# Optimization experiments

Measured on AMD Instinct MI355X. Metric: run time of the kernel, lower is better.

Reference implementation:

```python
import jax, jax.numpy as jnp
import numpy as np

B, N, NAB, NF, NG = 2, 512, 128, 128, 32
CUTOFF = 5.0


def ssp(x):
    # shifted softplus: ln(1+e^x) - ln 2
    return jax.nn.softplus(x) - jnp.log(2.0).astype(x.dtype)


def setup_inputs() -> dict:
    key = jax.random.key(0)
    ks = jax.random.split(key, 10)
    offsets = jnp.linspace(0.0, CUTOFF, NG)
    widths = jnp.full((NG,), offsets[1] - offsets[0])
    s = 0.05
    return {
        "r": jax.random.normal(ks[0], (B, N, NAB), jnp.float32),
        "e": jax.random.uniform(ks[1], (B, N, N), jnp.float32),
        "A": jax.random.uniform(ks[2], (B, N, N), jnp.float32),
        "offsets": offsets,
        "widths": widths,
        "W_df1": jax.random.normal(ks[3], (NG, NG), jnp.float32) * s,
        "b_df1": jnp.zeros((NG,), jnp.float32),
        "W_df2": jax.random.normal(ks[4], (NG, NF), jnp.float32) * s,
        "b_df2": jnp.zeros((NF,), jnp.float32),
        "W_af": jax.random.normal(ks[5], (NAB, NF), jnp.float32) * s,
        "W_d1": jax.random.normal(ks[6], (NF, NAB), jnp.float32) * s,
        "b_d1": jnp.zeros((NAB,), jnp.float32),
        "W_d2": jax.random.normal(ks[7], (NAB, NAB), jnp.float32) * s,
        "b_d2": jnp.zeros((NAB,), jnp.float32),
    }


def reference(r, e, A, offsets, widths, W_df1, b_df1, W_df2, b_df2,
              W_af, W_d1, b_d1, W_d2, b_d2):
    # Gaussian smearing (trainable offsets/widths, non-centered)
    coeff = -0.5 / (widths ** 2)                       # [G]
    diff = e[:, :, :, None] - offsets[None, None, None, :]  # [B,N,N,G]
    es = jnp.exp(coeff * diff ** 2)                    # [B,N,N,G]
    # DistanceFilter1 output is computed then discarded (faithful to source)
    _ = ssp(es @ W_df1 + b_df1)
    W = es @ W_df2 + b_df2                             # [B,N,N,F]
    rf = r @ W_af                                      # [B,N,F]
    # cfconv: broadcast-multiply-reduce over neighbor axis j
    y = jnp.einsum("bjf,bij,bijf->bif", rf, A, W)      # [B,N,F]
    y = ssp(y @ W_d1 + b_d1)                           # [B,N,NAB]
    y = y @ W_d2 + b_d2                                # [B,N,NAB]
    return y
```

## Files before the change

kernel.cpp:

```cpp
#include <hip/hip_runtime.h>
#include <math.h>

#define BB 2
#define NN 512
#define NAB 128
#define NF 128
#define NG 32

typedef _Float16 f16;
typedef f16 f16x8 __attribute__((ext_vector_type(8)));
typedef f16 f16x4 __attribute__((ext_vector_type(4)));
typedef f16 f16x2 __attribute__((ext_vector_type(2)));
typedef float f32x4 __attribute__((ext_vector_type(4)));

#define TS 520
#define SS 132

__global__ __launch_bounds__(256) void prep_rf(const float* __restrict__ r,
                                               const float* __restrict__ W_af,
                                               const float* __restrict__ W_d1,
                                               const float* __restrict__ W_d2,
                                               f16* __restrict__ rfT,
                                               f16* __restrict__ W1T,
                                               f16* __restrict__ W2T) {
    const int tid = threadIdx.x;
    const int r0  = blockIdx.x * 2;
    const int b   = r0 >> 9;
    const int j0  = r0 & 511;

    if (blockIdx.x < 32) {
        const int m  = blockIdx.x >> 4;
        const float* Wsrc = m ? W_d2 : W_d1;
        f16* Wdst = m ? W2T : W1T;
        const int k0 = (blockIdx.x & 15) * 8 + (tid >> 7) * 4;
        const int f  = tid & 127;
        f16x4 v;
        #pragma unroll
        for (int t = 0; t < 4; ++t) v[t] = (f16)Wsrc[(k0 + t) * NAB + f];
        *(f16x4*)(Wdst + f * NAB + k0) = v;
    }

    __shared__ float sr[2][128];
    __shared__ f16   st[128][2];

    if (tid < 256) {
        const int rr = tid >> 7, ff = tid & 127;
        sr[rr][ff] = r[(r0 + rr) * NAB + ff];
    }
    __syncthreads();

    const int f  = tid & 127;
    const int rh = tid >> 7;
    float a0 = 0.f;
    #pragma unroll 8
    for (int k = 0; k < NAB; ++k)
        a0 += sr[rh][k] * W_af[k * NF + f];
    st[f][rh] = (f16)a0;
    __syncthreads();

    if (tid < 128)
        *(f16x2*)(rfT + b * (NF * NN) + tid * NN + j0) = *(f16x2*)st[tid];
}

__global__ __launch_bounds__(256, 4) void fused_kernel(
    const float* __restrict__ e, const float* __restrict__ A,
    const f16*  __restrict__ rfT,
    const f16*  __restrict__ W1T, const f16* __restrict__ W2T,
    const float* __restrict__ offsets, const float* __restrict__ widths,
    const float* __restrict__ W_df2, const float* __restrict__ b_df2,
    const float* __restrict__ b_d1,  const float* __restrict__ b_d2,
    float* __restrict__ out) {

    const int bi  = blockIdx.x;
    const int b   = bi >> 9;
    const int tid = threadIdx.x;
    const int w    = tid >> 6;
    const int lane = tid & 63;
    const int q    = lane >> 4;
    const int n    = lane & 15;

    __shared__ __align__(16) float smem[2 * 33 * SS];
    __shared__ float sconst[64];
    __shared__ float sh1[128];
    __shared__ __align__(16) f16 yh16[128];
    __shared__ __align__(16) f16 hh16[128];

    f16* Tsh = (f16*)smem;

    if (tid < NG) {
        sconst[tid] = offsets[tid];
        const float wd = widths[tid];
        sconst[32 + tid] = -0.5f / (wd * wd);
    }

    const int j0 = (tid & 127) * 4;
    const float4 ev = *(const float4*)(e + bi * NN + j0);
    const float4 av = *(const float4*)(A + bi * NN + j0);
    __syncthreads();

    #pragma unroll
    for (int i = 0; i < 16; ++i) {
        const int g = (tid >> 7) + 2 * i;
        const float off = sconst[g];
        const float cf  = sconst[32 + g];
        const float d0 = ev.x - off, d1 = ev.y - off;
        const float d2 = ev.z - off, d3 = ev.w - off;
        f16x4 v;
        v[0] = (f16)(av.x * __expf(cf * d0 * d0));
        v[1] = (f16)(av.y * __expf(cf * d1 * d1));
        v[2] = (f16)(av.z * __expf(cf * d2 * d2));
        v[3] = (f16)(av.w * __expf(cf * d3 * d3));
        *(f16x4*)(Tsh + g * TS + j0) = v;
    }
    if (tid < 128) {
        f16x4 v;
        v[0] = (f16)av.x; v[1] = (f16)av.y; v[2] = (f16)av.z; v[3] = (f16)av.w;
        *(f16x4*)(Tsh + 32 * TS + j0) = v;
    }
    __syncthreads();

    const int kh = w >> 1;
    const int nh = w & 1;

    f32x4 acc[3][4];
    #pragma unroll
    for (int mt = 0; mt < 3; ++mt)
        #pragma unroll
        for (int nt = 0; nt < 4; ++nt)
            acc[mt][nt] = (f32x4){0.f, 0.f, 0.f, 0.f};

    const f16* Abase  = Tsh + n * TS + kh * 256 + q * 8;
    const f16* A2base = Tsh + 32 * TS + kh * 256 + q * 8;
    const f16* Bbase  = rfT + (size_t)b * (NF * NN) + (nh * 64 + n) * NN + kh * 256 + q * 8;

    #pragma unroll
    for (int kk = 0; kk < 8; ++kk) {
        f16x8 bc[4];
        #pragma unroll
        for (int nt = 0; nt < 4; ++nt)
            bc[nt] = *(const f16x8*)(Bbase + kk * 32 + nt * 16 * NN);
        const f16x8 a0 = *(const f16x8*)(Abase + kk * 32);
        const f16x8 a1 = *(const f16x8*)(Abase + 16 * TS + kk * 32);
        const f16x8 a2 = *(const f16x8*)(A2base + kk * 32);
        #pragma unroll
        for (int nt = 0; nt < 4; ++nt) {
            acc[0][nt] = __builtin_amdgcn_mfma_f32_16x16x32_f16(a0, bc[nt], acc[0][nt], 0, 0, 0);
            acc[1][nt] = __builtin_amdgcn_mfma_f32_16x16x32_f16(a1, bc[nt], acc[1][nt], 0, 0, 0);
            acc[2][nt] = __builtin_amdgcn_mfma_f32_16x16x32_f16(a2, bc[nt], acc[2][nt], 0, 0, 0);
        }
    }

    __syncthreads();
    float* Sp = smem + kh * (33 * SS);
    #pragma unroll
    for (int mt = 0; mt < 2; ++mt)
        #pragma unroll
        for (int nt = 0; nt < 4; ++nt)
            #pragma unroll
            for (int rr = 0; rr < 4; ++rr)
                Sp[(mt * 16 + q * 4 + rr) * SS + nh * 64 + nt * 16 + n] = acc[mt][nt][rr];
    if (q == 0) {
        #pragma unroll
        for (int nt = 0; nt < 4; ++nt)
            Sp[32 * SS + nh * 64 + nt * 16 + n] = acc[2][nt][0];
    }
    __syncthreads();

    if (tid < 128) {
        const float* S0 = smem;
        const float* S1 = smem + 33 * SS;
        float a = b_df2[tid] * (S0[32 * SS + tid] + S1[32 * SS + tid]);
        #pragma unroll 8
        for (int g = 0; g < NG; ++g)
            a += W_df2[g * NF + tid] * (S0[g * SS + tid] + S1[g * SS + tid]);
        yh16[tid] = (f16)a;
    }
    __syncthreads();

    f32x4 m1[2];
    m1[0] = (f32x4){0.f, 0.f, 0.f, 0.f};
    m1[1] = (f32x4){0.f, 0.f, 0.f, 0.f};
    #pragma unroll
    for (int kk = 0; kk < 4; ++kk) {
        const f16x8 af = *(const f16x8*)(yh16 + kk * 32 + q * 8);
        #pragma unroll
        for (int nt = 0; nt < 2; ++nt) {
            const f16x8 bf = *(const f16x8*)(W1T + (w * 32 + nt * 16 + n) * NAB + kk * 32 + q * 8);
            m1[nt] = __builtin_amdgcn_mfma_f32_16x16x32_f16(af, bf, m1[nt], 0, 0, 0);
        }
    }
    if (lane < 16) {
        sh1[w * 32 + 0  + lane] = m1[0][0];
        sh1[w * 32 + 16 + lane] = m1[1][0];
    }
    __syncthreads();

    if (tid < 128) {
        const float x = sh1[tid] + b_d1[tid];
        const float sp = (x > 0.f) ? (x + log1pf(__expf(-x))) : log1pf(__expf(x));
        hh16[tid] = (f16)(sp - 0.69314718055994530942f);
    }
    __syncthreads();

    f32x4 m2[2];
    m2[0] = (f32x4){0.f, 0.f, 0.f, 0.f};
    m2[1] = (f32x4){0.f, 0.f, 0.f, 0.f};
    #pragma unroll
    for (int kk = 0; kk < 4; ++kk) {
        const f16x8 af = *(const f16x8*)(hh16 + kk * 32 + q * 8);
        #pragma unroll
        for (int nt = 0; nt < 2; ++nt) {
            const f16x8 bf = *(const f16x8*)(W2T + (w * 32 + nt * 16 + n) * NAB + kk * 32 + q * 8);
            m2[nt] = __builtin_amdgcn_mfma_f32_16x16x32_f16(af, bf, m2[nt], 0, 0, 0);
        }
    }
    if (lane < 16) {
        const int f0 = w * 32 + lane;
        out[bi * NAB + f0]      = m2[0][0] + b_d2[f0];
        out[bi * NAB + f0 + 16] = m2[1][0] + b_d2[f0 + 16];
    }
}

extern "C" void kernel_launch(void* const* d_in, const int* in_sizes, int n_in,
                              void* d_out, int out_size, void* d_ws, size_t ws_size,
                              hipStream_t stream) {
    const float* r       = (const float*)d_in[0];
    const float* e       = (const float*)d_in[1];
    const float* A       = (const float*)d_in[2];
    const float* offsets = (const float*)d_in[3];
    const float* widths  = (const float*)d_in[4];
    const float* W_df2   = (const float*)d_in[7];
    const float* b_df2   = (const float*)d_in[8];
    const float* W_af    = (const float*)d_in[9];
    const float* W_d1    = (const float*)d_in[10];
    const float* b_d1    = (const float*)d_in[11];
    const float* W_d2    = (const float*)d_in[12];
    const float* b_d2    = (const float*)d_in[13];
    float* out = (float*)d_out;

    f16* rfT = (f16*)d_ws;
    f16* W1T = rfT + BB * NF * NN;
    f16* W2T = W1T + NAB * NAB;

    prep_rf<<<BB * NN / 2, 256, 0, stream>>>(r, W_af, W_d1, W_d2, rfT, W1T, W2T);
    fused_kernel<<<BB * NN, 256, 0, stream>>>(e, A, rfT, W1T, W2T,
                                              offsets, widths, W_df2, b_df2,
                                              b_d1, b_d2, out);
}
```

Before: 111.5 us.

## Process two atom rows per block to reuse rfT B-fragments

Each block of the fused kernel now handles two consecutive atoms i, sharing the rfT operand loads from global memory across both rows' MFMA accumulations and doubling the per-block weight reuse in the dense layers. The grid halves to 512 blocks and LDS doubles, with launch bounds relaxed to 2 blocks per CU. This trades occupancy and register pressure (96 accumulator vectors) for fewer global B loads and more MFMA work per load.

```diff
diff --git a/kernel.cpp b/kernel.cpp
--- a/kernel.cpp
+++ b/kernel.cpp
@@ -43,7 +43,7 @@
     __shared__ float sr[2][128];
     __shared__ f16   st[128][2];
 
-    if (tid < 256) {
+    {
         const int rr = tid >> 7, ff = tid & 127;
         sr[rr][ff] = r[(r0 + rr) * NAB + ff];
     }
@@ -62,7 +62,7 @@
         *(f16x2*)(rfT + b * (NF * NN) + tid * NN + j0) = *(f16x2*)st[tid];
 }
 
-__global__ __launch_bounds__(256, 4) void fused_kernel(
+__global__ __launch_bounds__(256, 2) void fused_kernel(
     const float* __restrict__ e, const float* __restrict__ A,
     const f16*  __restrict__ rfT,
     const f16*  __restrict__ W1T, const f16* __restrict__ W2T,
@@ -71,21 +71,22 @@
     const float* __restrict__ b_d1,  const float* __restrict__ b_d2,
     float* __restrict__ out) {
 
-    const int bi  = blockIdx.x;
-    const int b   = bi >> 9;
+    const int gi0 = blockIdx.x * 2;
+    const int b   = gi0 >> 9;
     const int tid = threadIdx.x;
     const int w    = tid >> 6;
     const int lane = tid & 63;
     const int q    = lane >> 4;
     const int n    = lane & 15;
 
-    __shared__ __align__(16) float smem[2 * 33 * SS];
+    __shared__ __align__(16) float smem[4 * 33 * SS];
     __shared__ float sconst[64];
-    __shared__ float sh1[128];
-    __shared__ __align__(16) f16 yh16[128];
-    __shared__ __align__(16) f16 hh16[128];
-
-    f16* Tsh = (f16*)smem;
+    __shared__ float sh1[2][128];
+    __shared__ __align__(16) f16 yh16[2][128];
+    __shared__ __align__(16) f16 hh16[2][128];
+
+    f16* Tsh0 = (f16*)smem;
+    f16* Tsh1 = Tsh0 + 33 * TS;
 
     if (tid < NG) {
         sconst[tid] = offsets[tid];
@@ -94,43 +95,63 @@
     }
 
     const int j0 = (tid & 127) * 4;
-    const float4 ev = *(const float4*)(e + bi * NN + j0);
-    const float4 av = *(const float4*)(A + bi * NN + j0);
-    __syncthreads();
-
-    #pragma unroll
-    for (int i = 0; i < 16; ++i) {
-        const int g = (tid >> 7) + 2 * i;
+    const float4 ev0 = *(const float4*)(e + (size_t)gi0 * NN + j0);
+    const float4 av0 = *(const float4*)(A + (size_t)gi0 * NN + j0);
+    const float4 ev1 = *(const float4*)(e + (size_t)(gi0 + 1) * NN + j0);
+    const float4 av1 = *(const float4*)(A + (size_t)(gi0 + 1) * NN + j0);
+    __syncthreads();
+
+    #pragma unroll
+    for (int it = 0; it < 16; ++it) {
+        const int g = (tid >> 7) + 2 * it;
         const float off = sconst[g];
         const float cf  = sconst[32 + g];
-        const float d0 = ev.x - off, d1 = ev.y - off;
-        const float d2 = ev.z - off, d3 = ev.w - off;
-        f16x4 v;
-        v[0] = (f16)(av.x * __expf(cf * d0 * d0));
-        v[1] = (f16)(av.y * __expf(cf * d1 * d1));
-        v[2] = (f16)(av.z * __expf(cf * d2 * d2));
-        v[3] = (f16)(av.w * __expf(cf * d3 * d3));
-        *(f16x4*)(Tsh + g * TS + j0) = v;
+        {
+            const float d0 = ev0.x - off, d1 = ev0.y - off;
+            const float d2 = ev0.z - off, d3 = ev0.w - off;
+            f16x4 v;
+            v[0] = (f16)(av0.x * __expf(cf * d0 * d0));
+            v[1] = (f16)(av0.y * __expf(cf * d1 * d1));
+            v[2] = (f16)(av0.z * __expf(cf * d2 * d2));
+            v[3] = (f16)(av0.w * __expf(cf * d3 * d3));
+            *(f16x4*)(Tsh0 + g * TS + j0) = v;
+        }
+        {
+            const float d0 = ev1.x - off, d1 = ev1.y - off;
+            const float d2 = ev1.z - off, d3 = ev1.w - off;
+            f16x4 v;
+            v[0] = (f16)(av1.x * __expf(cf * d0 * d0));
+            v[1] = (f16)(av1.y * __expf(cf * d1 * d1));
+            v[2] = (f16)(av1.z * __expf(cf * d2 * d2));
+            v[3] = (f16)(av1.w * __expf(cf * d3 * d3));
+            *(f16x4*)(Tsh1 + g * TS + j0) = v;
+        }
     }
     if (tid < 128) {
-        f16x4 v;
-        v[0] = (f16)av.x; v[1] = (f16)av.y; v[2] = (f16)av.z; v[3] = (f16)av.w;
-        *(f16x4*)(Tsh + 32 * TS + j0) = v;
+        f16x4 v0, v1;
+        v0[0] = (f16)av0.x; v0[1] = (f16)av0.y; v0[2] = (f16)av0.z; v0[3] = (f16)av0.w;
+        v1[0] = (f16)av1.x; v1[1] = (f16)av1.y; v1[2] = (f16)av1.z; v1[3] = (f16)av1.w;
+        *(f16x4*)(Tsh0 + 32 * TS + j0) = v0;
+        *(f16x4*)(Tsh1 + 32 * TS + j0) = v1;
     }
     __syncthreads();
 
     const int kh = w >> 1;
     const int nh = w & 1;
 
-    f32x4 acc[3][4];
-    #pragma unroll
-    for (int mt = 0; mt < 3; ++mt)
-        #pragma unroll
-        for (int nt = 0; nt < 4; ++nt)
-            acc[mt][nt] = (f32x4){0.f, 0.f, 0.f, 0.f};
-
-    const f16* Abase  = Tsh + n * TS + kh * 256 + q * 8;
-    const f16* A2base = Tsh + 32 * TS + kh * 256 + q * 8;
+    f32x4 acc[2][3][4];
+    #pragma unroll
+    for (int ii = 0; ii < 2; ++ii)
+        #pragma unroll
+        for (int mt = 0; mt < 3; ++mt)
+            #pragma unroll
+            for (int nt = 0; nt < 4; ++nt)
+                acc[ii][mt][nt] = (f32x4){0.f, 0.f, 0.f, 0.f};
+
+    const f16* A0base = Tsh0 + n * TS + kh * 256 + q * 8;
+    const f16* A0brow = Tsh0 + 32 * TS + kh * 256 + q * 8;
+    const f16* A1base = Tsh1 + n * TS + kh * 256 + q * 8;
+    const f16* A1brow = Tsh1 + 32 * TS + kh * 256 + q * 8;
     const f16* Bbase  = rfT + (size_t)b * (NF * NN) + (nh * 64 + n) * NN + kh * 256 + q * 8;
 
     #pragma unroll
@@ -139,85 +160,114 @@
         #pragma unroll
         for (int nt = 0; nt < 4; ++nt)
             bc[nt] = *(const f16x8*)(Bbase + kk * 32 + nt * 16 * NN);
-        const f16x8 a0 = *(const f16x8*)(Abase + kk * 32);
-        const f16x8 a1 = *(const f16x8*)(Abase + 16 * TS + kk * 32);
-        const f16x8 a2 = *(const f16x8*)(A2base + kk * 32);
+        const f16x8 a00 = *(const f16x8*)(A0base + kk * 32);
+        const f16x8 a01 = *(const f16x8*)(A0base + 16 * TS + kk * 32);
+        const f16x8 a02 = *(const f16x8*)(A0brow + kk * 32);
+        const f16x8 a10 = *(const f16x8*)(A1base + kk * 32);
+        const f16x8 a11 = *(const f16x8*)(A1base + 16 * TS + kk * 32);
+        const f16x8 a12 = *(const f16x8*)(A1brow + kk * 32);
         #pragma unroll
         for (int nt = 0; nt < 4; ++nt) {
-            acc[0][nt] = __builtin_amdgcn_mfma_f32_16x16x32_f16(a0, bc[nt], acc[0][nt], 0, 0, 0);
-            acc[1][nt] = __builtin_amdgcn_mfma_f32_16x16x32_f16(a1, bc[nt], acc[1][nt], 0, 0, 0);
-            acc[2][nt] = __builtin_amdgcn_mfma_f32_16x16x32_f16(a2, bc[nt], acc[2][nt], 0, 0, 0);
-        }
-    }
-
-    __syncthreads();
-    float* Sp = smem + kh * (33 * SS);
-    #pragma unroll
-    for (int mt = 0; mt < 2; ++mt)
-        #pragma unroll
-        for (int nt = 0; nt < 4; ++nt)
+            acc[0][0][nt] = __builtin_amdgcn_mfma_f32_16x16x32_f16(a00, bc[nt], acc[0][0][nt], 0, 0, 0);
+            acc[0][1][nt] = __builtin_amdgcn_mfma_f32_16x16x32_f16(a01, bc[nt], acc[0][1][nt], 0, 0, 0);
+            acc[0][2][nt] = __builtin_amdgcn_mfma_f32_16x16x32_f16(a02, bc[nt], acc[0][2][nt], 0, 0, 0);
+            acc[1][0][nt] = __builtin_amdgcn_mfma_f32_16x16x32_f16(a10, bc[nt], acc[1][0][nt], 0, 0, 0);
+            acc[1][1][nt] = __builtin_amdgcn_mfma_f32_16x16x32_f16(a11, bc[nt], acc[1][1][nt], 0, 0, 0);
+            acc[1][2][nt] = __builtin_amdgcn_mfma_f32_16x16x32_f16(a12, bc[nt], acc[1][2][nt], 0, 0, 0);
+        }
+    }
+
+    __syncthreads();
+    #pragma unroll
+    for (int ii = 0; ii < 2; ++ii) {
+        float* Sp = smem + (ii * 2 + kh) * (33 * SS);
+        #pragma unroll
+        for (int mt = 0; mt < 2; ++mt)
             #pragma unroll
-            for (int rr = 0; rr < 4; ++rr)
-                Sp[(mt * 16 + q * 4 + rr) * SS + nh * 64 + nt * 16 + n] = acc[mt][nt][rr];
-    if (q == 0) {
-        #pragma unroll
-        for (int nt = 0; nt < 4; ++nt)
-            Sp[32 * SS + nh * 64 + nt * 16 + n] = acc[2][nt][0];
-    }
-    __syncthreads();
-
-    if (tid < 128) {
-        const float* S0 = smem;
-        const float* S1 = smem + 33 * SS;
-        float a = b_df2[tid] * (S0[32 * SS + tid] + S1[32 * SS + tid]);
+            for (int nt = 0; nt < 4; ++nt)
+                #pragma unroll
+                for (int rr = 0; rr < 4; ++rr)
+                    Sp[(mt * 16 + q * 4 + rr) * SS + nh * 64 + nt * 16 + n] = acc[ii][mt][nt][rr];
+        if (q == 0) {
+            #pragma unroll
+            for (int nt = 0; nt < 4; ++nt)
+                Sp[32 * SS + nh * 64 + nt * 16 + n] = acc[ii][2][nt][0];
+        }
+    }
+    __syncthreads();
+
+    {
+        const int ii = tid >> 7;
+        const int f  = tid & 127;
+        const float* S0 = smem + (ii * 2 + 0) * (33 * SS);
+        const float* S1 = smem + (ii * 2 + 1) * (33 * SS);
+        float a = b_df2[f] * (S0[32 * SS + f] + S1[32 * SS + f]);
         #pragma unroll 8
         for (int g = 0; g < NG; ++g)
-            a += W_df2[g * NF + tid] * (S0[g * SS + tid] + S1[g * SS + tid]);
-        yh16[tid] = (f16)a;
-    }
-    __syncthreads();
-
-    f32x4 m1[2];
-    m1[0] = (f32x4){0.f, 0.f, 0.f, 0.f};
-    m1[1] = (f32x4){0.f, 0.f, 0.f, 0.f};
+            a += W_df2[g * NF + f] * (S0[g * SS + f] + S1[g * SS + f]);
+        yh16[ii][f] = (f16)a;
+    }
+    __syncthreads();
+
+    f32x4 m1[2][2];
+    #pragma unroll
+    for (int ii = 0; ii < 2; ++ii)
+        #pragma unroll
+        for (int nt = 0; nt < 2; ++nt)
+            m1[ii][nt] = (f32x4){0.f, 0.f, 0.f, 0.f};
     #pragma unroll
     for (int kk = 0; kk < 4; ++kk) {
-        const f16x8 af = *(const f16x8*)(yh16 + kk * 32 + q * 8);
+        const f16x8 af0 = *(const f16x8*)(yh16[0] + kk * 32 + q * 8);
+        const f16x8 af1 = *(const f16x8*)(yh16[1] + kk * 32 + q * 8);
         #pragma unroll
         for (int nt = 0; nt < 2; ++nt) {
             const f16x8 bf = *(const f16x8*)(W1T + (w * 32 + nt * 16 + n) * NAB + kk * 32 + q * 8);
-            m1[nt] = __builtin_amdgcn_mfma_f32_16x16x32_f16(af, bf, m1[nt], 0, 0, 0);
+            m1[0][nt] = __builtin_amdgcn_mfma_f32_16x16x32_f16(af0, bf, m1[0][nt], 0, 0, 0);
+            m1[1][nt] = __builtin_amdgcn_mfma_f32_16x16x32_f16(af1, bf, m1[1][nt], 0, 0, 0);
         }
     }
     if (lane < 16) {
-        sh1[w * 32 + 0  + lane] = m1[0][0];
-        sh1[w * 32 + 16 + lane] = m1[1][0];
-    }
-    __syncthreads();
-
-    if (tid < 128) {
-        const float x = sh1[tid] + b_d1[tid];
+        #pragma unroll
+        for (int ii = 0; ii < 2; ++ii) {
+            sh1[ii][w * 32 + 0  + lane] = m1[ii][0][0];
+            sh1[ii][w * 32 + 16 + lane] = m1[ii][1][0];
+        }
+    }
+    __syncthreads();
+
+    {
+        const int ii = tid >> 7;
+        const int f  = tid & 127;
+        const float x = sh1[ii][f] + b_d1[f];
         const float sp = (x > 0.f) ? (x + log1pf(__expf(-x))) : log1pf(__expf(x));
-        hh16[tid] = (f16)(sp - 0.69314718055994530942f);
-    }
-    __syncthreads();
-
-    f32x4 m2[2];
-    m2[0] = (f32x4){0.f, 0.f, 0.f, 0.f};
-    m2[1] = (f32x4){0.f, 0.f, 0.f, 0.f};
+        hh16[ii][f] = (f16)(sp - 0.69314718055994530942f);
+    }
+    __syncthreads();
+
+    f32x4 m2[2][2];
+    #pragma unroll
+    for (int ii = 0; ii < 2; ++ii)
+        #pragma unroll
+        for (int nt = 0; nt < 2; ++nt)
+            m2[ii][nt] = (f32x4){0.f, 0.f, 0.f, 0.f};
     #pragma unroll
     for (int kk = 0; kk < 4; ++kk) {
-        const f16x8 af = *(const f16x8*)(hh16 + kk * 32 + q * 8);
+        const f16x8 af0 = *(const f16x8*)(hh16[0] + kk * 32 + q * 8);
+        const f16x8 af1 = *(const f16x8*)(hh16[1] + kk * 32 + q * 8);
         #pragma unroll
         for (int nt = 0; nt < 2; ++nt) {
             const f16x8 bf = *(const f16x8*)(W2T + (w * 32 + nt * 16 + n) * NAB + kk * 32 + q * 8);
-            m2[nt] = __builtin_amdgcn_mfma_f32_16x16x32_f16(af, bf, m2[nt], 0, 0, 0);
+            m2[0][nt] = __builtin_amdgcn_mfma_f32_16x16x32_f16(af0, bf, m2[0][nt], 0, 0, 0);
+            m2[1][nt] = __builtin_amdgcn_mfma_f32_16x16x32_f16(af1, bf, m2[1][nt], 0, 0, 0);
         }
     }
     if (lane < 16) {
         const int f0 = w * 32 + lane;
-        out[bi * NAB + f0]      = m2[0][0] + b_d2[f0];
-        out[bi * NAB + f0 + 16] = m2[1][0] + b_d2[f0 + 16];
+        #pragma unroll
+        for (int ii = 0; ii < 2; ++ii) {
+            out[(size_t)(gi0 + ii) * NAB + f0]      = m2[ii][0][0] + b_d2[f0];
+            out[(size_t)(gi0 + ii) * NAB + f0 + 16] = m2[ii][1][0] + b_d2[f0 + 16];
+        }
     }
 }
 
@@ -243,7 +293,7 @@
     f16* W2T = W1T + NAB * NAB;
 
     prep_rf<<<BB * NN / 2, 256, 0, stream>>>(r, W_af, W_d1, W_d2, rfT, W1T, W2T);
-    fused_kernel<<<BB * NN, 256, 0, stream>>>(e, A, rfT, W1T, W2T,
-                                              offsets, widths, W_df2, b_df2,
-                                              b_d1, b_d2, out);
+    fused_kernel<<<BB * NN / 2, 256, 0, stream>>>(e, A, rfT, W1T, W2T,
+                                                  offsets, widths, W_df2, b_df2,
+                                                  b_d1, b_d2, out);
 }
```

After: 103.7 us. 7.0% less time.
